# Kernel tuning notes

Measured on AMD Instinct MI355X. Metric: run time of the kernel, lower is better.

## Reference

```python
import jax, jax.numpy as jnp
import numpy as np

EPS = 1e-5
NUM_HEAD = 8
D_MODEL = 512
D_K = D_MODEL // NUM_HEAD
SCALE = np.float32(1.0 / np.sqrt(D_K))


def _ln(x, g, b):
    m = jnp.mean(x, axis=-1, keepdims=True)
    v = jnp.var(x, axis=-1, keepdims=True)
    return g * (x - m) * jax.lax.rsqrt(v + EPS) + b


def setup_inputs() -> dict:
    key = jax.random.key(0)
    ks = jax.random.split(key, 24)
    B, W, S, V, D = 16, 256, 16, 32, D_MODEL
    DF = 2 * D
    w = lambda k, shape: (jax.random.normal(k, shape, jnp.float32) * 0.02)
    inp = {
        "text": jax.random.normal(ks[0], (B, W, D), jnp.float32),
        "av_feat": jax.random.normal(ks[1], (B, S, V, D), jnp.float32),
        "text_mask": jnp.ones((B, W, W), dtype=bool),
        "attn_sent_index": jnp.sort(jax.random.randint(ks[2], (B, W), 0, S), axis=-1),
        # res1 LayerNorm
        "ln_res1_g": jnp.ones((D,), jnp.float32), "ln_res1_b": jnp.zeros((D,), jnp.float32),
        # self-attention projections
        "sa_wq": w(ks[3], (D, D)), "sa_bq": jnp.zeros((D,), jnp.float32),
        "sa_wk": w(ks[4], (D, D)), "sa_bk": jnp.zeros((D,), jnp.float32),
        "sa_wv": w(ks[5], (D, D)), "sa_bv": jnp.zeros((D,), jnp.float32),
        "sa_wo": w(ks[6], (D, D)), "sa_bo": jnp.zeros((D,), jnp.float32),
        # cross-attention norms + projections
        "ca_ln_text_g": jnp.ones((D,), jnp.float32), "ca_ln_text_b": jnp.zeros((D,), jnp.float32),
        "ca_ln_av_g": jnp.ones((D,), jnp.float32), "ca_ln_av_b": jnp.zeros((D,), jnp.float32),
        "ca_wq": w(ks[7], (D, D)), "ca_bq": jnp.zeros((D,), jnp.float32),
        "ca_wk": w(ks[8], (D, D)), "ca_bk": jnp.zeros((D,), jnp.float32),
        "ca_wv": w(ks[9], (D, D)), "ca_bv": jnp.zeros((D,), jnp.float32),
        # post-cross norms
        "ln1_g": jnp.ones((D,), jnp.float32), "ln1_b": jnp.zeros((D,), jnp.float32),
        "ln2_g": jnp.ones((D,), jnp.float32), "ln2_b": jnp.zeros((D,), jnp.float32),
        # res2 LayerNorm + FFN (d_ff = 2*d_model per source)
        "ln_res2_g": jnp.ones((D,), jnp.float32), "ln_res2_b": jnp.zeros((D,), jnp.float32),
        "ff_w1": w(ks[10], (D, DF)), "ff_b1": jnp.zeros((DF,), jnp.float32),
        "ff_w2": w(ks[11], (DF, D)), "ff_b2": jnp.zeros((D,), jnp.float32),
    }
    return inp


def reference(text, av_feat, text_mask, attn_sent_index,
              ln_res1_g, ln_res1_b,
              sa_wq, sa_bq, sa_wk, sa_bk, sa_wv, sa_bv, sa_wo, sa_bo,
              ca_ln_text_g, ca_ln_text_b, ca_ln_av_g, ca_ln_av_b,
              ca_wq, ca_bq, ca_wk, ca_bk, ca_wv, ca_bv,
              ln1_g, ln1_b, ln2_g, ln2_b,
              ln_res2_g, ln_res2_b, ff_w1, ff_b1, ff_w2, ff_b2):
    B, W, D = text.shape
    S, V = av_feat.shape[1], av_feat.shape[2]

    # ---- res1: x + self_attn(norm(x)) (dropout = identity in eval) ----
    x = _ln(text, ln_res1_g, ln_res1_b)
    q = (x @ sa_wq + sa_bq).reshape(B, W, NUM_HEAD, D_K)
    k = (x @ sa_wk + sa_bk).reshape(B, W, NUM_HEAD, D_K)
    v = (x @ sa_wv + sa_bv).reshape(B, W, NUM_HEAD, D_K)
    scores = jnp.einsum('bqhd,bkhd->bhqk', q, k) * SCALE
    scores = jnp.where(text_mask[:, None, :, :], scores, jnp.float32(-1e9))
    a = jax.nn.softmax(scores, axis=-1)
    sa = jnp.einsum('bhqk,bkhd->bqhd', a, v).reshape(B, W, D) @ sa_wo + sa_bo
    text = text + sa

    # ---- cross attention: index-gathered sigmoid attention ----
    tn = _ln(text, ca_ln_text_g, ca_ln_text_b)
    an = _ln(av_feat, ca_ln_av_g, ca_ln_av_b)
    cq = (tn @ ca_wq + ca_bq).reshape(B, W, 1, NUM_HEAD, D_K)
    ck = (an @ ca_wk + ca_bk).reshape(B, S, V, NUM_HEAD, D_K)
    cv = (an @ ca_wv + ca_bv).reshape(B, S, V, NUM_HEAD, D_K)
    bidx = jnp.arange(B)[:, None]
    ck = ck[bidx, attn_sent_index]  # [B, W, V, H, Dk]
    cv = cv[bidx, attn_sent_index]  # [B, W, V, H, Dk]
    att = jax.nn.sigmoid(jnp.sum(cq * ck, axis=-1, keepdims=True) * SCALE)  # [B,W,V,H,1]
    res = jnp.sum(att * cv, axis=-3).reshape(B, W, D)

    text = _ln(text, ln1_g, ln1_b) + _ln(res, ln2_g, ln2_b)  # av_weight = 1

    # ---- res2: x + FFN(norm(x)) ----
    y = _ln(text, ln_res2_g, ln_res2_b)
    text = text + (jax.nn.relu(y @ ff_w1 + ff_b1) @ ff_w2 + ff_b2)

    attn_out = jnp.mean(att, axis=-2)[..., 0]  # mean over heads -> [B, W, V]
    return (text, attn_out)
```

## Files before the change

kernel.cpp:

```cpp
#include <hip/hip_runtime.h>
#include <hip/hip_bf16.h>


#define D_MODEL 512
#define NUM_HEAD 8
#define SCALE 0.125f
#define EPS 1e-5f

typedef __hip_bfloat16 bf16;
typedef __attribute__((ext_vector_type(8))) short short8;
typedef __attribute__((ext_vector_type(4))) float floatx4;

static __device__ __forceinline__ float s2f(short u) {
    unsigned int x = ((unsigned int)(unsigned short)u) << 16;
    float f; __builtin_memcpy(&f, &x, 4); return f;
}
static __device__ __forceinline__ short f2s(float f) {
    bf16 t = __float2bfloat16(f);
    short s; __builtin_memcpy(&s, &t, 2); return s;
}

static __device__ __forceinline__ void gload16(const short* g, short* l) {
    __builtin_amdgcn_global_load_lds(
        (const __attribute__((address_space(1))) unsigned int*)g,
        (__attribute__((address_space(3))) unsigned int*)l, 16, 0, 0);
}

struct TransArgs {
    const float* src[9];
    bf16* dst[9];
    int K[9], N[9];
    int start[10];
};

static __device__ __forceinline__ void ln_body(const float* __restrict__ inp,
                                               const float* __restrict__ g,
                                               const float* __restrict__ bta,
                                               bf16* __restrict__ out,
                                               size_t row, int t) {
    const float x0 = inp[row * D_MODEL + t];
    const float x1 = inp[row * D_MODEL + t + 256];
    float s = x0 + x1, sq = x0 * x0 + x1 * x1;
    #pragma unroll
    for (int off = 32; off >= 1; off >>= 1) {
        s += __shfl_xor(s, off, 64);
        sq += __shfl_xor(sq, off, 64);
    }
    __shared__ float ws_[4], wq_[4];
    if ((t & 63) == 0) { ws_[t >> 6] = s; wq_[t >> 6] = sq; }
    __syncthreads();
    s = ws_[0] + ws_[1] + ws_[2] + ws_[3];
    sq = wq_[0] + wq_[1] + wq_[2] + wq_[3];
    const float m = s * (1.f / D_MODEL);
    const float var = sq * (1.f / D_MODEL) - m * m;
    const float r = rsqrtf(var + EPS);
    out[row * D_MODEL + t]       = __float2bfloat16(g[t]       * (x0 - m) * r + bta[t]);
    out[row * D_MODEL + t + 256] = __float2bfloat16(g[t + 256] * (x1 - m) * r + bta[t + 256]);
}

__global__ __launch_bounds__(256) void ln_kernel(const float* __restrict__ inp,
                                                 const float* __restrict__ g,
                                                 const float* __restrict__ bta,
                                                 bf16* __restrict__ out) {
    ln_body(inp, g, bta, out, blockIdx.x, threadIdx.x);
}

__global__ __launch_bounds__(256) void prologue_kernel(TransArgs a, int nT,
                                                       const float* __restrict__ text,
                                                       const float* __restrict__ g1,
                                                       const float* __restrict__ b1,
                                                       bf16* __restrict__ xln,
                                                       const float* __restrict__ av,
                                                       const float* __restrict__ g2,
                                                       const float* __restrict__ b2,
                                                       bf16* __restrict__ an) {
    const int bid = blockIdx.x;
    if (bid >= nT) {
        const int r = bid - nT;
        if (r < 4096) ln_body(text, g1, b1, xln, r, threadIdx.x);
        else          ln_body(av, g2, b2, an, r - 4096, threadIdx.x);
        return;
    }
    int m = 0;
    while (bid >= a.start[m + 1]) m++;
    const int t = bid - a.start[m];
    const int N = a.N[m], K = a.K[m];
    const int tilesX = N >> 5;
    const int tx = t % tilesX, ty = t / tilesX;
    __shared__ bf16 tile[32][33];
    const int tid = threadIdx.x;
    const int r = tid >> 3, c0 = (tid & 7) * 4;
    const float* sp = a.src[m] + (size_t)(ty * 32 + r) * N + tx * 32 + c0;
    float4 v = *(const float4*)sp;
    tile[r][c0 + 0] = __float2bfloat16(v.x);
    tile[r][c0 + 1] = __float2bfloat16(v.y);
    tile[r][c0 + 2] = __float2bfloat16(v.z);
    tile[r][c0 + 3] = __float2bfloat16(v.w);
    __syncthreads();
    bf16* dp = a.dst[m] + (size_t)(tx * 32 + r) * K + ty * 32 + c0;
    #pragma unroll
    for (int i = 0; i < 4; i++) dp[i] = tile[c0 + i][r];
}

__global__ __launch_bounds__(256) void ln2_add_ln_kernel(const float* __restrict__ a,
                                                         const float* __restrict__ c,
                                                         const float* __restrict__ g1,
                                                         const float* __restrict__ b1,
                                                         const float* __restrict__ g2,
                                                         const float* __restrict__ b2,
                                                         const float* __restrict__ g3,
                                                         const float* __restrict__ b3,
                                                         float* __restrict__ text2,
                                                         bf16* __restrict__ y) {
    const size_t row = blockIdx.x;
    const int t = threadIdx.x;
    const float a0 = a[row * D_MODEL + t], a1 = a[row * D_MODEL + t + 256];
    const float c0 = c[row * D_MODEL + t], c1 = c[row * D_MODEL + t + 256];
    float sa = a0 + a1, qa = a0 * a0 + a1 * a1;
    float sc = c0 + c1, qc = c0 * c0 + c1 * c1;
    #pragma unroll
    for (int off = 32; off >= 1; off >>= 1) {
        sa += __shfl_xor(sa, off, 64); qa += __shfl_xor(qa, off, 64);
        sc += __shfl_xor(sc, off, 64); qc += __shfl_xor(qc, off, 64);
    }
    __shared__ float r_[4][4];
    if ((t & 63) == 0) { int w = t >> 6; r_[0][w] = sa; r_[1][w] = qa; r_[2][w] = sc; r_[3][w] = qc; }
    __syncthreads();
    sa = r_[0][0] + r_[0][1] + r_[0][2] + r_[0][3];
    qa = r_[1][0] + r_[1][1] + r_[1][2] + r_[1][3];
    sc = r_[2][0] + r_[2][1] + r_[2][2] + r_[2][3];
    qc = r_[3][0] + r_[3][1] + r_[3][2] + r_[3][3];
    const float ma = sa * (1.f / D_MODEL), mc = sc * (1.f / D_MODEL);
    const float ra = rsqrtf(qa * (1.f / D_MODEL) - ma * ma + EPS);
    const float rc = rsqrtf(qc * (1.f / D_MODEL) - mc * mc + EPS);
    const float v0 = g1[t] * (a0 - ma) * ra + b1[t] + g2[t] * (c0 - mc) * rc + b2[t];
    const float v1 = g1[t + 256] * (a1 - ma) * ra + b1[t + 256]
                   + g2[t + 256] * (c1 - mc) * rc + b2[t + 256];
    text2[row * D_MODEL + t] = v0;
    text2[row * D_MODEL + t + 256] = v1;
    float sv = v0 + v1, qv = v0 * v0 + v1 * v1;
    #pragma unroll
    for (int off = 32; off >= 1; off >>= 1) {
        sv += __shfl_xor(sv, off, 64); qv += __shfl_xor(qv, off, 64);
    }
    __syncthreads();
    if ((t & 63) == 0) { int w = t >> 6; r_[0][w] = sv; r_[1][w] = qv; }
    __syncthreads();
    sv = r_[0][0] + r_[0][1] + r_[0][2] + r_[0][3];
    qv = r_[1][0] + r_[1][1] + r_[1][2] + r_[1][3];
    const float mv = sv * (1.f / D_MODEL);
    const float rv = rsqrtf(qv * (1.f / D_MODEL) - mv * mv + EPS);
    y[row * D_MODEL + t]       = __float2bfloat16(g3[t]       * (v0 - mv) * rv + b3[t]);
    y[row * D_MODEL + t + 256] = __float2bfloat16(g3[t + 256] * (v1 - mv) * rv + b3[t + 256]);
}

template <int BN>
static __device__ __forceinline__ void mfma_loop(const short* __restrict__ Ag,
                                                 const short* __restrict__ Bg,
                                                 int m0, int n0, int K,
                                                 short* As, short* Bs,
                                                 floatx4* acc ) {
    constexpr int NI = BN / 32;
    const int tid = threadIdx.x, lane = tid & 63, w = tid >> 6;
    const int quad = lane >> 4, l15 = lane & 15;
    const int wm = (w >> 1) * 64, wn = (w & 1) * (BN / 2);
    const int sr = lane >> 3;
    const int sc = (((lane & 7) ^ sr) & 7) * 8;
    const int rsw = (l15 & 7) << 3;

    #define STAGE(buf, kk0)                                                         \
        do {                                                                        \
            short* Ad = As + (buf) * (128 * 64);                                    \
            short* Bd = Bs + (buf) * (BN * 64);                                     \
            _Pragma("unroll")                                                       \
            for (int p = 0; p < 4; p++) {                                           \
                const int rb = w * 32 + p * 8;                                      \
                gload16(&Ag[(size_t)(m0 + rb + sr) * K + (kk0) + sc], &Ad[rb * 64]);\
            }                                                                       \
            _Pragma("unroll")                                                       \
            for (int p = 0; p < BN / 32; p++) {                                     \
                const int rb = w * (BN / 4) + p * 8;                                \
                gload16(&Bg[(size_t)(n0 + rb + sr) * K + (kk0) + sc], &Bd[rb * 64]);\
            }                                                                       \
        } while (0)

    STAGE(0, 0);
    __syncthreads();
    int cur = 0;
    for (int kk0 = 0; kk0 < K; kk0 += 64) {
        const bool more = (kk0 + 64 < K);
        if (more) STAGE(cur ^ 1, kk0 + 64);
        const short* Ac = As + cur * (128 * 64);
        const short* Bc = Bs + cur * (BN * 64);
        __builtin_amdgcn_s_setprio(1);
        #pragma unroll
        for (int ks = 0; ks < 2; ks++) {
            const int kc = (ks * 32 + quad * 8) ^ rsw;
            short8 bfr[NI];
            #pragma unroll
            for (int ni = 0; ni < NI; ni++)
                bfr[ni] = *(const short8*)&Bc[(wn + ni * 16 + l15) * 64 + kc];
            #pragma unroll
            for (int mi = 0; mi < 4; mi++) {
                short8 am = *(const short8*)&Ac[(wm + mi * 16 + l15) * 64 + kc];
                #pragma unroll
                for (int ni = 0; ni < NI; ni++)
                    acc[mi * NI + ni] = __builtin_amdgcn_mfma_f32_16x16x32_bf16(
                        am, bfr[ni], acc[mi * NI + ni], 0, 0, 0);
            }
        }
        __builtin_amdgcn_s_setprio(0);
        if (more) __syncthreads();
        cur ^= 1;
    }
    #undef STAGE
}

template <int BN, int RES, bool RELU, bool OUT_BF16>
__global__ __launch_bounds__(256) void gemm128(const bf16* __restrict__ A,
                                               const bf16* __restrict__ BT,
                                               const float* __restrict__ bias,
                                               const float* __restrict__ resid,
                                               void* __restrict__ C,
                                               int M, int Ntot, int K) {
    constexpr int NI = BN / 32;
    __shared__ __align__(16) short As[2 * 128 * 64];
    __shared__ __align__(16) short Bs[2 * BN * 64];
    const int nx = gridDim.x;
    const int nwg = nx * gridDim.y;
    int lin = blockIdx.y * nx + blockIdx.x;
    if ((nwg & 7) == 0) lin = (lin & 7) * (nwg >> 3) + (lin >> 3);
    const int m0 = (lin / nx) * 128, n0 = (lin % nx) * BN;
    floatx4 acc[4 * NI] = {};
    mfma_loop<BN>((const short*)A, (const short*)BT, m0, n0, K, As, Bs, acc);
    const int tid = threadIdx.x, lane = tid & 63, w = tid >> 6;
    const int quad = lane >> 4, l15 = lane & 15;
    const int wm = (w >> 1) * 64, wn = (w & 1) * (BN / 2);
    #pragma unroll
    for (int mi = 0; mi < 4; mi++)
        #pragma unroll
        for (int ni = 0; ni < NI; ni++)
            #pragma unroll
            for (int r = 0; r < 4; r++) {
                const int row = m0 + wm + mi * 16 + quad * 4 + r;
                const int col = n0 + wn + ni * 16 + l15;
                float v = acc[mi * NI + ni][r] + bias[col];
                if (RELU) v = fmaxf(v, 0.f);
                if (RES == 1) v += resid[(size_t)row * Ntot + col];
                if (OUT_BF16) ((bf16*)C)[(size_t)row * Ntot + col] = __float2bfloat16(v);
                else          ((float*)C)[(size_t)row * Ntot + col] = v;
            }
}

__global__ __launch_bounds__(256) void gemm_qkv_kv(const bf16* __restrict__ xln,
                                                   const bf16* __restrict__ wqT,
                                                   const float* __restrict__ bq,
                                                   const float* __restrict__ bk,
                                                   const float* __restrict__ bv,
                                                   bf16* __restrict__ qkv,
                                                   const bf16* __restrict__ an,
                                                   const bf16* __restrict__ cwkT,
                                                   const float* __restrict__ cbk,
                                                   const float* __restrict__ cbv,
                                                   bf16* __restrict__ kvb) {
    __shared__ __align__(16) short As[2 * 128 * 64];
    __shared__ __align__(16) short Bs[2 * 128 * 64];
    const int bid0 = blockIdx.x;
    const int bid = (bid0 & 7) * 112 + (bid0 >> 3);
    const bf16 *A_, *B_;
    const float *p0, *p1, *p2;
    bf16* Cg;
    int Ntot, m0, n0;
    if (bid < 384) {
        A_ = xln; B_ = wqT; p0 = bq; p1 = bk; p2 = bv; Cg = qkv;
        Ntot = 1536; m0 = (bid / 12) * 128; n0 = (bid % 12) * 128;
    } else {
        const int r = bid - 384;
        A_ = an; B_ = cwkT; p0 = cbk; p1 = cbv; p2 = cbv; Cg = kvb;
        Ntot = 1024; m0 = (r / 8) * 128; n0 = (r % 8) * 128;
    }
    floatx4 acc[16] = {};
    mfma_loop<128>((const short*)A_, (const short*)B_, m0, n0, 512, As, Bs, acc);
    const int tid = threadIdx.x, lane = tid & 63, w = tid >> 6;
    const int quad = lane >> 4, l15 = lane & 15;
    const int wm = (w >> 1) * 64, wn = (w & 1) * 64;
    const int seg = n0 >> 9;
    const float* bias = (seg == 0) ? p0 : ((seg == 1) ? p1 : p2);
    #pragma unroll
    for (int mi = 0; mi < 4; mi++)
        #pragma unroll
        for (int ni = 0; ni < 4; ni++)
            #pragma unroll
            for (int r = 0; r < 4; r++) {
                const int row = m0 + wm + mi * 16 + quad * 4 + r;
                const int col = n0 + wn + ni * 16 + l15;
                Cg[(size_t)row * Ntot + col] =
                    __float2bfloat16(acc[mi * 4 + ni][r] + bias[col & 511]);
            }
}

__global__ __launch_bounds__(256) void self_attn_mfma(const bf16* __restrict__ q,
                                                      const bf16* __restrict__ k,
                                                      const bf16* __restrict__ v,
                                                      int ld,
                                                      bf16* __restrict__ sa) {
    const int qc = blockIdx.x, h = blockIdx.y, b = blockIdx.z;
    const int tid = threadIdx.x, lane = tid & 63, w = tid >> 6;
    const int quad = lane >> 4, l15 = lane & 15;
    __shared__ __align__(16) short Kt[64 * 72];
    __shared__ __align__(16) short VT[64 * 72];
    __shared__ __align__(16) short Ps[4][16 * 72];
    const int qrow = b * 256 + qc * 64 + w * 16 + l15;
    const short* qg = (const short*)q + (size_t)qrow * ld + h * 64;
    short8 qf0 = *(const short8*)&qg[quad * 8];
    short8 qf1 = *(const short8*)&qg[32 + quad * 8];
    floatx4 o[4] = {};
    float den[4] = {};
    for (int kt0 = 0; kt0 < 256; kt0 += 64) {
        __syncthreads();
        {
            const int row = tid >> 2, c0 = (tid & 3) * 16;
            const short* kg = (const short*)k + (size_t)(b * 256 + kt0 + row) * ld + h * 64 + c0;
            *(short8*)&Kt[row * 72 + c0]     = *(const short8*)kg;
            *(short8*)&Kt[row * 72 + c0 + 8] = *(const short8*)(kg + 8);
        }
        {
            const int key = tid & 63, dk0 = (tid >> 6) * 16;
            const short* vg = (const short*)v + (size_t)(b * 256 + kt0 + key) * ld + h * 64 + dk0;
            short8 v0 = *(const short8*)vg;
            short8 v1 = *(const short8*)(vg + 8);
            #pragma unroll
            for (int i = 0; i < 8; i++) VT[(dk0 + i) * 72 + key] = v0[i];
            #pragma unroll
            for (int i = 0; i < 8; i++) VT[(dk0 + 8 + i) * 72 + key] = v1[i];
        }
        __syncthreads();
        floatx4 sacc[4] = {};
        #pragma unroll
        for (int ni = 0; ni < 4; ni++) {
            short8 b0 = *(const short8*)&Kt[(ni * 16 + l15) * 72 + quad * 8];
            short8 b1 = *(const short8*)&Kt[(ni * 16 + l15) * 72 + 32 + quad * 8];
            sacc[ni] = __builtin_amdgcn_mfma_f32_16x16x32_bf16(qf0, b0, sacc[ni], 0, 0, 0);
            sacc[ni] = __builtin_amdgcn_mfma_f32_16x16x32_bf16(qf1, b1, sacc[ni], 0, 0, 0);
        }
        #pragma unroll
        for (int ni = 0; ni < 4; ni++)
            #pragma unroll
            for (int r = 0; r < 4; r++) {
                const float e = __expf(sacc[ni][r] * SCALE);
                den[r] += e;
                Ps[w][(quad * 4 + r) * 72 + ni * 16 + l15] = f2s(e);
            }
        #pragma unroll
        for (int kc = 0; kc < 2; kc++) {
            short8 af = *(const short8*)&Ps[w][l15 * 72 + kc * 32 + quad * 8];
            #pragma unroll
            for (int ni = 0; ni < 4; ni++) {
                short8 bv = *(const short8*)&VT[(ni * 16 + l15) * 72 + kc * 32 + quad * 8];
                o[ni] = __builtin_amdgcn_mfma_f32_16x16x32_bf16(af, bv, o[ni], 0, 0, 0);
            }
        }
    }
    #pragma unroll
    for (int off = 1; off < 16; off <<= 1)
        #pragma unroll
        for (int r = 0; r < 4; r++) den[r] += __shfl_xor(den[r], off, 64);
    float inv[4];
    #pragma unroll
    for (int r = 0; r < 4; r++) inv[r] = 1.f / den[r];
    const int qo = b * 256 + qc * 64 + w * 16 + quad * 4;
    #pragma unroll
    for (int ni = 0; ni < 4; ni++)
        #pragma unroll
        for (int r = 0; r < 4; r++)
            sa[(size_t)(qo + r) * D_MODEL + h * 64 + ni * 16 + l15] =
                __float2bfloat16(o[ni][r] * inv[r]);
}

__global__ __launch_bounds__(256) void cross_attn3(const bf16* __restrict__ kv,
                                                   const bf16* __restrict__ cq,
                                                   const int* __restrict__ sidx,
                                                   float* __restrict__ res,
                                                   float* __restrict__ out_attn) {
    const int s = blockIdx.x, b = blockIdx.y, t = threadIdx.x;
    __shared__ int wrange[2];
    __shared__ __align__(16) short Ks[32 * 576];
    __shared__ __align__(16) short Vs[32 * 576];
    __shared__ __align__(16) short qs[32 * 576];
    __shared__ float att[32 * 256];
    if (t == 0) { wrange[0] = 256; wrange[1] = 0; }
    __syncthreads();
    const int* sb = sidx + b * 256;
    {
        const int sv = sb[t];
        if (sv == s) {
            if (t == 0 || sb[t - 1] != s) wrange[0] = t;
            if (t == 255 || sb[t + 1] != s) wrange[1] = t + 1;
        }
    }
    {
        const int v = t >> 3, hh = t & 7;
        const short* kg = (const short*)kv + ((size_t)((b * 16 + s) * 32 + v)) * 1024 + hh * 64;
        const short* vg = kg + 512;
        short* kd = &Ks[v * 576 + hh * 72];
        short* vd = &Vs[v * 576 + hh * 72];
        #pragma unroll
        for (int c = 0; c < 8; c++) {
            *(short8*)&kd[c * 8] = *(const short8*)&kg[c * 8];
            *(short8*)&vd[c * 8] = *(const short8*)&vg[c * 8];
        }
    }
    __syncthreads();
    const int w0 = wrange[0], w1 = wrange[1];
    const int h2 = t >> 5, dp = t & 31;
    const short* cqg = (const short*)cq;
    for (int wc = w0; wc < w1; wc += 32) {
        const int len = (w1 - wc < 32) ? (w1 - wc) : 32;
        for (int i = t; i < len * 64; i += 256) {
            const int e = i * 8;
            const int row = e >> 9, col = e & 511;
            *(short8*)&qs[row * 576 + (col >> 6) * 72 + (col & 63)] =
                *(const short8*)&cqg[((size_t)(b * 256 + wc + row)) * 512 + col];
        }
        __syncthreads();
        for (int i = t; i < len * 256; i += 256) {
            const int wl = i >> 8, r = i & 255, v = r >> 3, h = r & 7;
            const short* qp = &qs[wl * 576 + h * 72];
            const short* kp = &Ks[v * 576 + h * 72];
            float dot = 0.f;
            #pragma unroll
            for (int c = 0; c < 8; c++) {
                short8 q8 = *(const short8*)&qp[c * 8];
                short8 k8 = *(const short8*)&kp[c * 8];
                dot += s2f(q8[0]) * s2f(k8[0]) + s2f(q8[1]) * s2f(k8[1])
                     + s2f(q8[2]) * s2f(k8[2]) + s2f(q8[3]) * s2f(k8[3])
                     + s2f(q8[4]) * s2f(k8[4]) + s2f(q8[5]) * s2f(k8[5])
                     + s2f(q8[6]) * s2f(k8[6]) + s2f(q8[7]) * s2f(k8[7]);
            }
            att[wl * 256 + r] = 1.f / (1.f + __expf(-dot * SCALE));
        }
        __syncthreads();
        for (int wl = 0; wl < len; wl++) {
            float r0 = 0.f, r1 = 0.f;
            #pragma unroll
            for (int vv = 0; vv < 32; ++vv) {
                const float av = att[wl * 256 + vv * 8 + h2];
                const int pv = *(const int*)&Vs[vv * 576 + h2 * 72 + dp * 2];
                r0 += av * s2f((short)(pv & 0xffff));
                r1 += av * s2f((short)(pv >> 16));
            }
            *(float2*)&res[((size_t)(b * 256 + wc + wl)) * 512 + h2 * 64 + dp * 2] =
                make_float2(r0, r1);
        }
        if (t < 32) {
            for (int wl = 0; wl < len; wl++) {
                float m = 0.f;
                #pragma unroll
                for (int j = 0; j < 8; j++) m += att[wl * 256 + t * 8 + j];
                out_attn[((size_t)(b * 256 + wc + wl)) * 32 + t] = m * 0.125f;
            }
        }
        __syncthreads();
    }
}

extern "C" void kernel_launch(void* const* d_in, const int* in_sizes, int n_in,
                              void* d_out, int out_size, void* d_ws, size_t ws_size,
                              hipStream_t stream) {
    const int B = 16, S = 16;
    const int M1 = 4096, M2 = 8192;

    const float* text = (const float*)d_in[0];
    const float* av   = (const float*)d_in[1];
    const int* sidx   = (const int*)d_in[3];
    const float* ln_res1_g = (const float*)d_in[4];
    const float* ln_res1_b = (const float*)d_in[5];
    const float* sa_wq = (const float*)d_in[6];
    const float* sa_bq = (const float*)d_in[7];
    const float* sa_wk = (const float*)d_in[8];
    const float* sa_bk = (const float*)d_in[9];
    const float* sa_wv = (const float*)d_in[10];
    const float* sa_bv = (const float*)d_in[11];
    const float* sa_wo = (const float*)d_in[12];
    const float* sa_bo = (const float*)d_in[13];
    const float* ca_ln_text_g = (const float*)d_in[14];
    const float* ca_ln_text_b = (const float*)d_in[15];
    const float* ca_ln_av_g = (const float*)d_in[16];
    const float* ca_ln_av_b = (const float*)d_in[17];
    const float* ca_wq = (const float*)d_in[18];
    const float* ca_bq = (const float*)d_in[19];
    const float* ca_wk = (const float*)d_in[20];
    const float* ca_bk = (const float*)d_in[21];
    const float* ca_wv = (const float*)d_in[22];
    const float* ca_bv = (const float*)d_in[23];
    const float* ln1_g = (const float*)d_in[24];
    const float* ln1_b = (const float*)d_in[25];
    const float* ln2_g = (const float*)d_in[26];
    const float* ln2_b = (const float*)d_in[27];
    const float* ln_res2_g = (const float*)d_in[28];
    const float* ln_res2_b = (const float*)d_in[29];
    const float* ff_w1 = (const float*)d_in[30];
    const float* ff_b1 = (const float*)d_in[31];
    const float* ff_w2 = (const float*)d_in[32];
    const float* ff_b2 = (const float*)d_in[33];

    char* wsb = (char*)d_ws;
    const size_t MBy = 1024 * 1024;
    bf16*  WT    = (bf16*)(wsb);
    bf16*  xln   = (bf16*)(wsb + 6 * MBy);
    bf16*  qkv   = (bf16*)(wsb + 10 * MBy);
    bf16*  sab   = (bf16*)(wsb + 22 * MBy);
    float* text1 = (float*)(wsb + 26 * MBy);
    bf16*  tn    = (bf16*)(wsb + 34 * MBy);
    bf16*  an    = (bf16*)(wsb + 38 * MBy);
    bf16*  cqb   = (bf16*)(wsb + 46 * MBy);
    bf16*  kvb   = (bf16*)(wsb + 50 * MBy);
    float* res   = (float*)(wsb + 66 * MBy);
    float* text2 = (float*)(wsb + 74 * MBy);
    bf16*  y     = (bf16*)(wsb + 82 * MBy);
    bf16*  h1    = (bf16*)(wsb + 86 * MBy);

    bf16* wqT  = WT;
    bf16* cwqT = WT + 1048576;
    bf16* cwkT = WT + 1310720;
    bf16* woT  = WT + 786432;
    bf16* f1T  = WT + 1835008;
    bf16* f2T  = WT + 2359296;

    float* out_text = (float*)d_out;
    float* out_attn = (float*)d_out + (size_t)M1 * D_MODEL;

    TransArgs ta;
    const float* srcs[9] = {sa_wq, sa_wk, sa_wv, sa_wo, ca_wq, ca_wk, ca_wv, ff_w1, ff_w2};
    bf16* dsts[9] = {wqT, WT + 262144, WT + 524288, woT, cwqT, cwkT, WT + 1572864, f1T, f2T};
    const int Ks_[9] = {512, 512, 512, 512, 512, 512, 512, 512, 1024};
    const int Ns_[9] = {512, 512, 512, 512, 512, 512, 512, 1024, 512};
    int cum = 0;
    for (int i = 0; i < 9; i++) {
        ta.src[i] = srcs[i]; ta.dst[i] = dsts[i]; ta.K[i] = Ks_[i]; ta.N[i] = Ns_[i];
        ta.start[i] = cum;
        cum += (Ks_[i] >> 5) * (Ns_[i] >> 5);
    }
    ta.start[9] = cum;

    const dim3 blk256(256);
    const dim3 gD(8, 32);
    const dim3 gF1(8, 32);

    prologue_kernel<<<cum + M1 + M2, blk256, 0, stream>>>(ta, cum,
                                                          text, ln_res1_g, ln_res1_b, xln,
                                                          av, ca_ln_av_g, ca_ln_av_b, an);
    gemm_qkv_kv<<<896, blk256, 0, stream>>>(xln, wqT, sa_bq, sa_bk, sa_bv, qkv,
                                            an, cwkT, ca_bk, ca_bv, kvb);
    self_attn_mfma<<<dim3(4, NUM_HEAD, B), blk256, 0, stream>>>(qkv, qkv + 512, qkv + 1024, 1536, sab);
    gemm128<64, 1, false, false><<<gD, blk256, 0, stream>>>(sab, woT, sa_bo, text, text1, M1, D_MODEL, D_MODEL);
    ln_kernel<<<M1, blk256, 0, stream>>>(text1, ca_ln_text_g, ca_ln_text_b, tn);
    gemm128<64, 0, false, true><<<gD, blk256, 0, stream>>>(tn, cwqT, ca_bq, nullptr, cqb, M1, D_MODEL, D_MODEL);
    cross_attn3<<<dim3(S, B), blk256, 0, stream>>>(kvb, cqb, sidx, res, out_attn);
    ln2_add_ln_kernel<<<M1, blk256, 0, stream>>>(text1, res, ln1_g, ln1_b, ln2_g, ln2_b,
                                                 ln_res2_g, ln_res2_b, text2, y);
    gemm128<128, 0, true, true><<<gF1, blk256, 0, stream>>>(y, f1T, ff_b1, nullptr, h1, M1, 1024, D_MODEL);
    gemm128<64, 1, false, false><<<gD, blk256, 0, stream>>>(h1, f2T, ff_b2, text2, out_text, M1, D_MODEL, 1024);
}
```

Before: 263.3 us.

## Fuse Wo/LN/cross-Q and LN2/FFN1 stages into cooperative grid-synced kernels

Replaces five separate launches (Wo GEMM, LN, cross-Q GEMM, double-LN, FFN1 GEMM) with two cooperative kernels that use grid.sync between phases, each on a 256-block grid. It aims to remove kernel launch gaps and tail effects between small dependent stages. In exchange it adds grid-wide barriers and fixes the grid at 256 blocks, so each block handles 16 LayerNorm rows serially, which may underuse the GPU in the LN phases.

Result: slower. 498.3 us (+89.3%).

```diff
diff --git a/kernel.cpp b/kernel.cpp
--- a/kernel.cpp
+++ b/kernel.cpp
@@ -1,5 +1,8 @@
 #include <hip/hip_runtime.h>
 #include <hip/hip_bf16.h>
+#include <hip/hip_cooperative_groups.h>
+
+namespace cg = cooperative_groups;
 
 
 #define D_MODEL 512
@@ -58,11 +61,55 @@
     out[row * D_MODEL + t + 256] = __float2bfloat16(g[t + 256] * (x1 - m) * r + bta[t + 256]);
 }
 
-__global__ __launch_bounds__(256) void ln_kernel(const float* __restrict__ inp,
-                                                 const float* __restrict__ g,
-                                                 const float* __restrict__ bta,
-                                                 bf16* __restrict__ out) {
-    ln_body(inp, g, bta, out, blockIdx.x, threadIdx.x);
+static __device__ __forceinline__ void ln2_row(const float* __restrict__ a,
+                                               const float* __restrict__ c,
+                                               const float* __restrict__ g1,
+                                               const float* __restrict__ b1,
+                                               const float* __restrict__ g2,
+                                               const float* __restrict__ b2,
+                                               const float* __restrict__ g3,
+                                               const float* __restrict__ b3,
+                                               float* __restrict__ text2,
+                                               bf16* __restrict__ y,
+                                               size_t row, int t) {
+    const float a0 = a[row * D_MODEL + t], a1 = a[row * D_MODEL + t + 256];
+    const float c0 = c[row * D_MODEL + t], c1 = c[row * D_MODEL + t + 256];
+    float sa = a0 + a1, qa = a0 * a0 + a1 * a1;
+    float sc = c0 + c1, qc = c0 * c0 + c1 * c1;
+    #pragma unroll
+    for (int off = 32; off >= 1; off >>= 1) {
+        sa += __shfl_xor(sa, off, 64); qa += __shfl_xor(qa, off, 64);
+        sc += __shfl_xor(sc, off, 64); qc += __shfl_xor(qc, off, 64);
+    }
+    __shared__ float r_[4][4];
+    if ((t & 63) == 0) { int w = t >> 6; r_[0][w] = sa; r_[1][w] = qa; r_[2][w] = sc; r_[3][w] = qc; }
+    __syncthreads();
+    sa = r_[0][0] + r_[0][1] + r_[0][2] + r_[0][3];
+    qa = r_[1][0] + r_[1][1] + r_[1][2] + r_[1][3];
+    sc = r_[2][0] + r_[2][1] + r_[2][2] + r_[2][3];
+    qc = r_[3][0] + r_[3][1] + r_[3][2] + r_[3][3];
+    const float ma = sa * (1.f / D_MODEL), mc = sc * (1.f / D_MODEL);
+    const float ra = rsqrtf(qa * (1.f / D_MODEL) - ma * ma + EPS);
+    const float rc = rsqrtf(qc * (1.f / D_MODEL) - mc * mc + EPS);
+    const float v0 = g1[t] * (a0 - ma) * ra + b1[t] + g2[t] * (c0 - mc) * rc + b2[t];
+    const float v1 = g1[t + 256] * (a1 - ma) * ra + b1[t + 256]
+                   + g2[t + 256] * (c1 - mc) * rc + b2[t + 256];
+    text2[row * D_MODEL + t] = v0;
+    text2[row * D_MODEL + t + 256] = v1;
+    float sv = v0 + v1, qv = v0 * v0 + v1 * v1;
+    #pragma unroll
+    for (int off = 32; off >= 1; off >>= 1) {
+        sv += __shfl_xor(sv, off, 64); qv += __shfl_xor(qv, off, 64);
+    }
+    __syncthreads();
+    if ((t & 63) == 0) { int w = t >> 6; r_[0][w] = sv; r_[1][w] = qv; }
+    __syncthreads();
+    sv = r_[0][0] + r_[0][1] + r_[0][2] + r_[0][3];
+    qv = r_[1][0] + r_[1][1] + r_[1][2] + r_[1][3];
+    const float mv = sv * (1.f / D_MODEL);
+    const float rv = rsqrtf(qv * (1.f / D_MODEL) - mv * mv + EPS);
+    y[row * D_MODEL + t]       = __float2bfloat16(g3[t]       * (v0 - mv) * rv + b3[t]);
+    y[row * D_MODEL + t + 256] = __float2bfloat16(g3[t + 256] * (v1 - mv) * rv + b3[t + 256]);
 }
 
 __global__ __launch_bounds__(256) void prologue_kernel(TransArgs a, int nT,
@@ -100,58 +147,6 @@
     bf16* dp = a.dst[m] + (size_t)(tx * 32 + r) * K + ty * 32 + c0;
     #pragma unroll
     for (int i = 0; i < 4; i++) dp[i] = tile[c0 + i][r];
-}
-
-__global__ __launch_bounds__(256) void ln2_add_ln_kernel(const float* __restrict__ a,
-                                                         const float* __restrict__ c,
-                                                         const float* __restrict__ g1,
-                                                         const float* __restrict__ b1,
-                                                         const float* __restrict__ g2,
-                                                         const float* __restrict__ b2,
-                                                         const float* __restrict__ g3,
-                                                         const float* __restrict__ b3,
-                                                         float* __restrict__ text2,
-                                                         bf16* __restrict__ y) {
-    const size_t row = blockIdx.x;
-    const int t = threadIdx.x;
-    const float a0 = a[row * D_MODEL + t], a1 = a[row * D_MODEL + t + 256];
-    const float c0 = c[row * D_MODEL + t], c1 = c[row * D_MODEL + t + 256];
-    float sa = a0 + a1, qa = a0 * a0 + a1 * a1;
-    float sc = c0 + c1, qc = c0 * c0 + c1 * c1;
-    #pragma unroll
-    for (int off = 32; off >= 1; off >>= 1) {
-        sa += __shfl_xor(sa, off, 64); qa += __shfl_xor(qa, off, 64);
-        sc += __shfl_xor(sc, off, 64); qc += __shfl_xor(qc, off, 64);
-    }
-    __shared__ float r_[4][4];
-    if ((t & 63) == 0) { int w = t >> 6; r_[0][w] = sa; r_[1][w] = qa; r_[2][w] = sc; r_[3][w] = qc; }
-    __syncthreads();
-    sa = r_[0][0] + r_[0][1] + r_[0][2] + r_[0][3];
-    qa = r_[1][0] + r_[1][1] + r_[1][2] + r_[1][3];
-    sc = r_[2][0] + r_[2][1] + r_[2][2] + r_[2][3];
-    qc = r_[3][0] + r_[3][1] + r_[3][2] + r_[3][3];
-    const float ma = sa * (1.f / D_MODEL), mc = sc * (1.f / D_MODEL);
-    const float ra = rsqrtf(qa * (1.f / D_MODEL) - ma * ma + EPS);
-    const float rc = rsqrtf(qc * (1.f / D_MODEL) - mc * mc + EPS);
-    const float v0 = g1[t] * (a0 - ma) * ra + b1[t] + g2[t] * (c0 - mc) * rc + b2[t];
-    const float v1 = g1[t + 256] * (a1 - ma) * ra + b1[t + 256]
-                   + g2[t + 256] * (c1 - mc) * rc + b2[t + 256];
-    text2[row * D_MODEL + t] = v0;
-    text2[row * D_MODEL + t + 256] = v1;
-    float sv = v0 + v1, qv = v0 * v0 + v1 * v1;
-    #pragma unroll
-    for (int off = 32; off >= 1; off >>= 1) {
-        sv += __shfl_xor(sv, off, 64); qv += __shfl_xor(qv, off, 64);
-    }
-    __syncthreads();
-    if ((t & 63) == 0) { int w = t >> 6; r_[0][w] = sv; r_[1][w] = qv; }
-    __syncthreads();
-    sv = r_[0][0] + r_[0][1] + r_[0][2] + r_[0][3];
-    qv = r_[1][0] + r_[1][1] + r_[1][2] + r_[1][3];
-    const float mv = sv * (1.f / D_MODEL);
-    const float rv = rsqrtf(qv * (1.f / D_MODEL) - mv * mv + EPS);
-    y[row * D_MODEL + t]       = __float2bfloat16(g3[t]       * (v0 - mv) * rv + b3[t]);
-    y[row * D_MODEL + t + 256] = __float2bfloat16(g3[t + 256] * (v1 - mv) * rv + b3[t + 256]);
 }
 
 template <int BN>
@@ -296,6 +291,116 @@
                 const int col = n0 + wn + ni * 16 + l15;
                 Cg[(size_t)row * Ntot + col] =
                     __float2bfloat16(acc[mi * 4 + ni][r] + bias[col & 511]);
+            }
+}
+
+__global__ __launch_bounds__(256) void wo_ln_cq(const bf16* __restrict__ sab,
+                                                const bf16* __restrict__ woT,
+                                                const float* __restrict__ bo,
+                                                const float* __restrict__ text,
+                                                float* __restrict__ text1,
+                                                const float* __restrict__ lng,
+                                                const float* __restrict__ lnb,
+                                                bf16* __restrict__ tn,
+                                                const bf16* __restrict__ cwqT,
+                                                const float* __restrict__ cbq,
+                                                bf16* __restrict__ cqb) {
+    __shared__ __align__(16) short As[2 * 128 * 64];
+    __shared__ __align__(16) short Bs[2 * 64 * 64];
+    cg::grid_group grid = cg::this_grid();
+    const int tid = threadIdx.x, lane = tid & 63, w = tid >> 6;
+    const int quad = lane >> 4, l15 = lane & 15;
+    const int wm = (w >> 1) * 64, wn = (w & 1) * 32;
+    const int bid0 = blockIdx.x;
+    const int lin = (bid0 & 7) * 32 + (bid0 >> 3);
+    const int m0 = (lin >> 3) * 128, n0 = (lin & 7) * 64;
+
+    {
+        floatx4 acc[8] = {};
+        mfma_loop<64>((const short*)sab, (const short*)woT, m0, n0, 512, As, Bs, acc);
+        #pragma unroll
+        for (int mi = 0; mi < 4; mi++)
+            #pragma unroll
+            for (int ni = 0; ni < 2; ni++)
+                #pragma unroll
+                for (int r = 0; r < 4; r++) {
+                    const int row = m0 + wm + mi * 16 + quad * 4 + r;
+                    const int col = n0 + wn + ni * 16 + l15;
+                    text1[(size_t)row * D_MODEL + col] =
+                        acc[mi * 2 + ni][r] + bo[col] + text[(size_t)row * D_MODEL + col];
+                }
+    }
+    __threadfence();
+    grid.sync();
+
+    for (int r = 0; r < 16; r++) {
+        ln_body(text1, lng, lnb, tn, (size_t)blockIdx.x * 16 + r, tid);
+        __syncthreads();
+    }
+    __threadfence();
+    grid.sync();
+
+    {
+        floatx4 acc[8] = {};
+        mfma_loop<64>((const short*)tn, (const short*)cwqT, m0, n0, 512, As, Bs, acc);
+        #pragma unroll
+        for (int mi = 0; mi < 4; mi++)
+            #pragma unroll
+            for (int ni = 0; ni < 2; ni++)
+                #pragma unroll
+                for (int r = 0; r < 4; r++) {
+                    const int row = m0 + wm + mi * 16 + quad * 4 + r;
+                    const int col = n0 + wn + ni * 16 + l15;
+                    cqb[(size_t)row * D_MODEL + col] =
+                        __float2bfloat16(acc[mi * 2 + ni][r] + cbq[col]);
+                }
+    }
+}
+
+__global__ __launch_bounds__(256) void ln2_ff1(const float* __restrict__ text1,
+                                               const float* __restrict__ res,
+                                               const float* __restrict__ g1,
+                                               const float* __restrict__ b1,
+                                               const float* __restrict__ g2,
+                                               const float* __restrict__ b2,
+                                               const float* __restrict__ g3,
+                                               const float* __restrict__ b3,
+                                               float* __restrict__ text2,
+                                               bf16* __restrict__ y,
+                                               const bf16* __restrict__ f1T,
+                                               const float* __restrict__ fb1,
+                                               bf16* __restrict__ h1) {
+    __shared__ __align__(16) short As[2 * 128 * 64];
+    __shared__ __align__(16) short Bs[2 * 128 * 64];
+    cg::grid_group grid = cg::this_grid();
+    const int tid = threadIdx.x;
+
+    for (int r = 0; r < 16; r++) {
+        ln2_row(text1, res, g1, b1, g2, b2, g3, b3, text2, y,
+                (size_t)blockIdx.x * 16 + r, tid);
+        __syncthreads();
+    }
+    __threadfence();
+    grid.sync();
+
+    const int lane = tid & 63, w = tid >> 6;
+    const int quad = lane >> 4, l15 = lane & 15;
+    const int wm = (w >> 1) * 64, wn = (w & 1) * 64;
+    const int bid0 = blockIdx.x;
+    const int lin = (bid0 & 7) * 32 + (bid0 >> 3);
+    const int m0 = (lin >> 3) * 128, n0 = (lin & 7) * 128;
+    floatx4 acc[16] = {};
+    mfma_loop<128>((const short*)y, (const short*)f1T, m0, n0, 512, As, Bs, acc);
+    #pragma unroll
+    for (int mi = 0; mi < 4; mi++)
+        #pragma unroll
+        for (int ni = 0; ni < 4; ni++)
+            #pragma unroll
+            for (int r = 0; r < 4; r++) {
+                const int row = m0 + wm + mi * 16 + quad * 4 + r;
+                const int col = n0 + wn + ni * 16 + l15;
+                h1[(size_t)row * 1024 + col] =
+                    __float2bfloat16(fmaxf(acc[mi * 4 + ni][r] + fb1[col], 0.f));
             }
 }
 
@@ -545,7 +650,6 @@
 
     const dim3 blk256(256);
     const dim3 gD(8, 32);
-    const dim3 gF1(8, 32);
 
     prologue_kernel<<<cum + M1 + M2, blk256, 0, stream>>>(ta, cum,
                                                           text, ln_res1_g, ln_res1_b, xln,
@@ -553,12 +657,29 @@
     gemm_qkv_kv<<<896, blk256, 0, stream>>>(xln, wqT, sa_bq, sa_bk, sa_bv, qkv,
                                             an, cwkT, ca_bk, ca_bv, kvb);
     self_attn_mfma<<<dim3(4, NUM_HEAD, B), blk256, 0, stream>>>(qkv, qkv + 512, qkv + 1024, 1536, sab);
-    gemm128<64, 1, false, false><<<gD, blk256, 0, stream>>>(sab, woT, sa_bo, text, text1, M1, D_MODEL, D_MODEL);
-    ln_kernel<<<M1, blk256, 0, stream>>>(text1, ca_ln_text_g, ca_ln_text_b, tn);
-    gemm128<64, 0, false, true><<<gD, blk256, 0, stream>>>(tn, cwqT, ca_bq, nullptr, cqb, M1, D_MODEL, D_MODEL);
+    {
+        const bf16* a_sab = sab; const bf16* a_woT = woT; const float* a_bo = sa_bo;
+        const float* a_text = text; float* a_text1 = text1;
+        const float* a_g = ca_ln_text_g; const float* a_b = ca_ln_text_b;
+        bf16* a_tn = tn; const bf16* a_cwqT = cwqT; const float* a_cbq = ca_bq;
+        bf16* a_cqb = cqb;
+        void* args[] = {&a_sab, &a_woT, &a_bo, &a_text, &a_text1, &a_g, &a_b,
+                        &a_tn, &a_cwqT, &a_cbq, &a_cqb};
+        hipLaunchCooperativeKernel(reinterpret_cast<void*>(wo_ln_cq),
+                                   dim3(256), blk256, args, 0, stream);
+    }
     cross_attn3<<<dim3(S, B), blk256, 0, stream>>>(kvb, cqb, sidx, res, out_attn);
-    ln2_add_ln_kernel<<<M1, blk256, 0, stream>>>(text1, res, ln1_g, ln1_b, ln2_g, ln2_b,
-                                                 ln_res2_g, ln_res2_b, text2, y);
-    gemm128<128, 0, true, true><<<gF1, blk256, 0, stream>>>(y, f1T, ff_b1, nullptr, h1, M1, 1024, D_MODEL);
+    {
+        const float* a_text1 = text1; const float* a_res = res;
+        const float* a_g1 = ln1_g; const float* a_b1 = ln1_b;
+        const float* a_g2 = ln2_g; const float* a_b2 = ln2_b;
+        const float* a_g3 = ln_res2_g; const float* a_b3 = ln_res2_b;
+        float* a_text2 = text2; bf16* a_y = y;
+        const bf16* a_f1T = f1T; const float* a_fb1 = ff_b1; bf16* a_h1 = h1;
+        void* args[] = {&a_text1, &a_res, &a_g1, &a_b1, &a_g2, &a_b2, &a_g3, &a_b3,
+                        &a_text2, &a_y, &a_f1T, &a_fb1, &a_h1};
+        hipLaunchCooperativeKernel(reinterpret_cast<void*>(ln2_ff1),
+                                   dim3(256), blk256, args, 0, stream);
+    }
     gemm128<64, 1, false, false><<<gD, blk256, 0, stream>>>(h1, f2T, ff_b2, text2, out_text, M1, D_MODEL, 1024);
 }
```
